# Kernel optimization log

Hardware: AMD Instinct MI355X
Metric: run time of the kernel (lower is better)

The kernel has to match this reference:

```python
import jax, jax.numpy as jnp
import numpy as np

B, C_IN, H, W = 128, 2, 64, 64
K = 50  # value-iteration steps


def _conv(x, w, b=None):
    # NCHW input, OIHW weights, stride 1, SAME padding (odd kernel)
    y = jax.lax.conv_general_dilated(
        x, w, window_strides=(1, 1), padding='SAME',
        dimension_numbers=('NCHW', 'OIHW', 'NCHW'))
    if b is not None:
        y = y + b[None, :, None, None]
    return y


def setup_inputs() -> dict:
    key = jax.random.key(0)
    ks = jax.random.split(key, 10)
    pos_x = jax.random.randint(ks[0], (B,), 0, H, dtype=jnp.int32)
    pos_y = jax.random.randint(ks[1], (B,), 0, W, dtype=jnp.int32)
    # channel 0 encodes agent position (single >0 entry); channel 1 is the obstacle/goal map
    ch0 = jnp.zeros((B, H, W), jnp.float32).at[jnp.arange(B), pos_x, pos_y].set(1.0)
    ch1 = jax.random.normal(ks[2], (B, H, W), jnp.float32)
    x = jnp.stack([ch0, ch1], axis=1)  # [B, 2, H, W]
    sc = lambda *s: 1.0 / np.sqrt(np.prod(s[1:])) if len(s) > 1 else 0.1
    h_w = jax.random.normal(ks[3], (150, C_IN, 3, 3), jnp.float32) * sc(150, C_IN, 3, 3)
    h_b = jax.random.normal(ks[4], (150,), jnp.float32) * 0.1
    r_w = jax.random.normal(ks[5], (1, 150, 3, 3), jnp.float32) * sc(1, 150, 3, 3)
    r_b = jax.random.normal(ks[6], (1,), jnp.float32) * 0.1
    q_w = jax.random.normal(ks[7], (10, 2, 3, 3), jnp.float32) * sc(10, 2, 3, 3)
    q_b = jax.random.normal(ks[8], (10,), jnp.float32) * 0.1
    fc_w = jax.random.normal(ks[9], (8, 10), jnp.float32) * sc(8, 10)
    return {'x': x, 'pos_x': pos_x, 'pos_y': pos_y,
            'h_w': h_w, 'h_b': h_b, 'r_w': r_w, 'r_b': r_b,
            'q_w': q_w, 'q_b': q_b, 'fc_w': fc_w}


def reference(x, pos_x, pos_y, h_w, h_b, r_w, r_b, q_w, q_b, fc_w):
    h = _conv(x, h_w, h_b)            # [B, 150, H, W]
    r = _conv(h, r_w, r_b)            # [B, 1, H, W]
    v0 = jnp.zeros_like(r)

    def vi_step(v, _):
        q = _conv(jnp.concatenate([r, v], axis=1), q_w, q_b)  # [B, 10, H, W]
        return jnp.max(q, axis=1, keepdims=True), None

    v, _ = jax.lax.scan(vi_step, v0, None, length=K)
    q = _conv(jnp.concatenate([r, v], axis=1), q_w, q_b)      # [B, 10, H, W]
    q_at = q[jnp.arange(q.shape[0]), :, pos_x, pos_y]         # [B, 10]
    return q_at @ fc_w.T                                       # [B, 8]
```

## Files before the change

### kernel.cpp

```cpp
#include <hip/hip_runtime.h>

#define K_ITERS 50

__global__ void vin_setup(const float* __restrict__ h_w, const float* __restrict__ h_b,
                          const float* __restrict__ r_w, float* __restrict__ ws) {
    int t = threadIdx.x;
    if (t < 162) {
        int i = t / 81, rem = t % 81, dq = rem / 9, ds = rem % 9;
        float s = 0.f;
        for (int m = 0; m < 150; ++m)
            s = fmaf(r_w[m * 9 + dq], h_w[(m * 2 + i) * 9 + ds], s);
        ws[t] = s;
    } else if (t < 171) {
        int dq = t - 162;
        float s = 0.f;
        for (int m = 0; m < 150; ++m)
            s = fmaf(r_w[m * 9 + dq], h_b[m], s);
        ws[t] = s;
    }
}

#define SR_OFF 9248
#define SW_OFF 13736
#define LDS_TOT 14178

__device__ __forceinline__ void vi_step(const float* __restrict__ cur, float* __restrict__ nxt,
                                        int row, int col0,
                                        const float (&qr)[10][8], const float (&qwv)[10][9]) {
    float nb[3][12];
#pragma unroll
    for (int dy = 0; dy < 3; ++dy) {
#pragma unroll
        for (int j = 0; j < 3; ++j) {
            float4 v = *(const float4*)&cur[(row + dy) * 68 + col0 + 4 * j];
            nb[dy][4 * j + 0] = v.x; nb[dy][4 * j + 1] = v.y;
            nb[dy][4 * j + 2] = v.z; nb[dy][4 * j + 3] = v.w;
        }
    }
    float vmax[8];
#pragma unroll
    for (int c = 0; c < 10; ++c) {
#pragma unroll
        for (int p = 0; p < 8; ++p) {
            float acc = qr[c][p];
#pragma unroll
            for (int ky = 0; ky < 3; ++ky)
#pragma unroll
                for (int kx = 0; kx < 3; ++kx)
                    acc = fmaf(qwv[c][ky * 3 + kx], nb[ky][p + kx], acc);
            vmax[p] = (c == 0) ? acc : fmaxf(vmax[p], acc);
        }
    }
#pragma unroll
    for (int p = 0; p < 8; ++p)
        nxt[(row + 1) * 68 + col0 + 1 + p] = vmax[p];
}

__launch_bounds__(512)
__global__ void vin_main(const float* __restrict__ x,
                         const int* __restrict__ pos_x, const int* __restrict__ pos_y,
                         const float* __restrict__ q_w, const float* __restrict__ q_b,
                         const float* __restrict__ fc_w, const float* __restrict__ r_b,
                         const float* __restrict__ ws, float* __restrict__ out) {
    __shared__ __align__(16) float S[LDS_TOT];
    const int tid = threadIdx.x;
    const int b = blockIdx.x;
    const int row = tid >> 3;
    const int col0 = (tid & 7) << 3;
    float* SW = S + SW_OFF;

    float4 z4 = make_float4(0.f, 0.f, 0.f, 0.f);
    for (int i = tid; i < 3434; i += 512) ((float4*)S)[i] = z4;
    for (int i = tid; i < 171; i += 512) SW[i] = ws[i];
    for (int i = tid; i < 180; i += 512) SW[171 + i] = q_w[i];
    if (tid < 10) SW[351 + tid] = q_b[tid];
    for (int i = tid; i < 80; i += 512) SW[361 + i] = fc_w[i];
    if (tid == 0) SW[441] = r_b[0];
    __syncthreads();

    {
        const float4* xg = (const float4*)(x + (size_t)b * 8192);
        for (int i = tid; i < 2048; i += 512) {
            float4 v = xg[i];
            int ch = i >> 10, rem = i & 1023;
            int y = rem >> 4, xc = (rem & 15) << 2;
            float* dst = S + ch * 4624 + (y + 2) * 68 + xc + 2;
            dst[0] = v.x; dst[1] = v.y; dst[2] = v.z; dst[3] = v.w;
        }
    }
    __syncthreads();

    {
        float xb0[5][12], xb1[5][12];
        const float* X0 = S;
        const float* X1 = S + 4624;
#pragma unroll
        for (int dy = 0; dy < 5; ++dy) {
#pragma unroll
            for (int j = 0; j < 3; ++j) {
                float4 a = *(const float4*)&X0[(row + dy) * 68 + col0 + 4 * j];
                xb0[dy][4 * j + 0] = a.x; xb0[dy][4 * j + 1] = a.y;
                xb0[dy][4 * j + 2] = a.z; xb0[dy][4 * j + 3] = a.w;
                float4 c = *(const float4*)&X1[(row + dy) * 68 + col0 + 4 * j];
                xb1[dy][4 * j + 0] = c.x; xb1[dy][4 * j + 1] = c.y;
                xb1[dy][4 * j + 2] = c.z; xb1[dy][4 * j + 3] = c.w;
            }
        }
        float racc[8];
        float rbv = SW[441];
#pragma unroll
        for (int p = 0; p < 8; ++p) racc[p] = rbv;
#pragma unroll
        for (int dqy = 0; dqy < 3; ++dqy) {
            bool rowok = (row + dqy >= 1) && (row + dqy <= 64);
#pragma unroll
            for (int dqx = 0; dqx < 3; ++dqx) {
                int dq = dqy * 3 + dqx;
                float rh = SW[162 + dq];
                float w20[9], w21[9];
#pragma unroll
                for (int ds = 0; ds < 9; ++ds) {
                    w20[ds] = SW[dq * 9 + ds];
                    w21[ds] = SW[81 + dq * 9 + ds];
                }
#pragma unroll
                for (int p = 0; p < 8; ++p) {
                    float t = rh;
#pragma unroll
                    for (int dsy = 0; dsy < 3; ++dsy)
#pragma unroll
                        for (int dsx = 0; dsx < 3; ++dsx) {
                            int ds = dsy * 3 + dsx;
                            t = fmaf(w20[ds], xb0[dqy + dsy][p + dqx + dsx], t);
                            t = fmaf(w21[ds], xb1[dqy + dsy][p + dqx + dsx], t);
                        }
                    int qx = col0 + p + dqx - 1;
                    bool ok = rowok && (qx >= 0) && (qx < 64);
                    racc[p] += ok ? t : 0.f;
                }
            }
        }
        float* SR = S + SR_OFF;
#pragma unroll
        for (int p = 0; p < 8; ++p)
            SR[(row + 1) * 68 + col0 + 1 + p] = racc[p];
    }
    __syncthreads();

    float qr[10][8];
    float qwv[10][9];
    {
        float rnb[3][12];
        const float* SR = S + SR_OFF;
#pragma unroll
        for (int dy = 0; dy < 3; ++dy) {
#pragma unroll
            for (int j = 0; j < 3; ++j) {
                float4 v = *(const float4*)&SR[(row + dy) * 68 + col0 + 4 * j];
                rnb[dy][4 * j + 0] = v.x; rnb[dy][4 * j + 1] = v.y;
                rnb[dy][4 * j + 2] = v.z; rnb[dy][4 * j + 3] = v.w;
            }
        }
#pragma unroll
        for (int c = 0; c < 10; ++c) {
            float qbc = SW[351 + c];
            float w[9];
#pragma unroll
            for (int j = 0; j < 9; ++j) w[j] = SW[171 + c * 18 + j];
#pragma unroll
            for (int p = 0; p < 8; ++p) {
                float acc = qbc;
#pragma unroll
                for (int ky = 0; ky < 3; ++ky)
#pragma unroll
                    for (int kx = 0; kx < 3; ++kx)
                        acc = fmaf(w[ky * 3 + kx], rnb[ky][p + kx], acc);
                qr[c][p] = acc;
            }
        }
#pragma unroll
        for (int c = 0; c < 10; ++c)
#pragma unroll
            for (int j = 0; j < 9; ++j) qwv[c][j] = SW[171 + c * 18 + 9 + j];
        for (int i = tid; i < 2312; i += 512) ((float4*)S)[i] = z4;
    }
    __syncthreads();

    float* vA = S;
    float* vB = S + 4624;
#pragma unroll 1
    for (int k = 0; k < K_ITERS / 2; ++k) {
        vi_step(vA, vB, row, col0, qr, qwv);
        __syncthreads();
        vi_step(vB, vA, row, col0, qr, qwv);
        __syncthreads();
    }

    int pr = pos_x[b], pc = pos_y[b];
    if (row == pr && (pc >> 3) == (tid & 7)) {
        int p = pc & 7;
        float qf[10];
#pragma unroll
        for (int c = 0; c < 10; ++c) {
            float acc = qr[c][p];
#pragma unroll
            for (int ky = 0; ky < 3; ++ky)
#pragma unroll
                for (int kx = 0; kx < 3; ++kx)
                    acc = fmaf(qwv[c][3 * ky + kx], vA[(pr + ky) * 68 + pc + kx], acc);
            qf[c] = acc;
        }
#pragma unroll
        for (int o = 0; o < 8; ++o) {
            float s = 0.f;
#pragma unroll
            for (int c = 0; c < 10; ++c) s = fmaf(SW[361 + o * 10 + c], qf[c], s);
            out[b * 8 + o] = s;
        }
    }
}

extern "C" void kernel_launch(void* const* d_in, const int* in_sizes, int n_in,
                              void* d_out, int out_size, void* d_ws, size_t ws_size,
                              hipStream_t stream) {
    const float* x     = (const float*)d_in[0];
    const int*   pos_x = (const int*)d_in[1];
    const int*   pos_y = (const int*)d_in[2];
    const float* h_w   = (const float*)d_in[3];
    const float* h_b   = (const float*)d_in[4];
    const float* r_w   = (const float*)d_in[5];
    const float* r_b   = (const float*)d_in[6];
    const float* q_w   = (const float*)d_in[7];
    const float* q_b   = (const float*)d_in[8];
    const float* fc_w  = (const float*)d_in[9];
    float* ws  = (float*)d_ws;
    float* out = (float*)d_out;

    vin_setup<<<1, 192, 0, stream>>>(h_w, h_b, r_w, ws);
    vin_main<<<128, 512, 0, stream>>>(x, pos_x, pos_y, q_w, q_b, fc_w, r_b, ws, out);
}
```

Baseline: 198.7 us.

## Split each image across two blocks with global-memory halo exchange per iteration

Each image is now processed by two workgroups, each owning 32 rows, so 256 blocks run instead of 128 and more CUs are occupied. Each thread computes 4 columns instead of 8. The two halves swap boundary rows through double-buffered global slots and synchronise every value-iteration step with acquire/release flag spin-waits. This adds inter-block synchronisation latency on every step, and correctness relies on both partner blocks being co-resident.

```diff
diff --git a/kernel.cpp b/kernel.cpp
--- a/kernel.cpp
+++ b/kernel.cpp
@@ -1,6 +1,16 @@
 #include <hip/hip_runtime.h>
 
-#define K_ITERS 50
+#define KI 50
+#define STR 72
+
+#define VA_OFF 0
+#define VB_OFF 2448
+#define X0_OFF 0
+#define R_OFF 4896
+#define X1_OFF 7344
+#define W_OFF 10080
+#define LDS_TOT 10522
+
 
 __global__ void vin_setup(const float* __restrict__ h_w, const float* __restrict__ h_b,
                           const float* __restrict__ r_w, float* __restrict__ ws) {
@@ -18,147 +28,132 @@
             s = fmaf(r_w[m * 9 + dq], h_b[m], s);
         ws[t] = s;
     }
+    int* flags = (int*)ws + 256;
+    if (t < 256) flags[t] = 0;
 }
 
-#define SR_OFF 9248
-#define SW_OFF 13736
-#define LDS_TOT 14178
-
-__device__ __forceinline__ void vi_step(const float* __restrict__ cur, float* __restrict__ nxt,
-                                        int row, int col0,
-                                        const float (&qr)[10][8], const float (&qwv)[10][9]) {
-    float nb[3][12];
-#pragma unroll
-    for (int dy = 0; dy < 3; ++dy) {
-#pragma unroll
-        for (int j = 0; j < 3; ++j) {
-            float4 v = *(const float4*)&cur[(row + dy) * 68 + col0 + 4 * j];
-            nb[dy][4 * j + 0] = v.x; nb[dy][4 * j + 1] = v.y;
-            nb[dy][4 * j + 2] = v.z; nb[dy][4 * j + 3] = v.w;
-        }
-    }
-    float vmax[8];
-#pragma unroll
-    for (int c = 0; c < 10; ++c) {
-#pragma unroll
-        for (int p = 0; p < 8; ++p) {
-            float acc = qr[c][p];
-#pragma unroll
-            for (int ky = 0; ky < 3; ++ky)
-#pragma unroll
-                for (int kx = 0; kx < 3; ++kx)
-                    acc = fmaf(qwv[c][ky * 3 + kx], nb[ky][p + kx], acc);
-            vmax[p] = (c == 0) ? acc : fmaxf(vmax[p], acc);
-        }
-    }
-#pragma unroll
-    for (int p = 0; p < 8; ++p)
-        nxt[(row + 1) * 68 + col0 + 1 + p] = vmax[p];
-}
-
-__launch_bounds__(512)
+__launch_bounds__(512, 2)
 __global__ void vin_main(const float* __restrict__ x,
                          const int* __restrict__ pos_x, const int* __restrict__ pos_y,
                          const float* __restrict__ q_w, const float* __restrict__ q_b,
                          const float* __restrict__ fc_w, const float* __restrict__ r_b,
-                         const float* __restrict__ ws, float* __restrict__ out) {
+                         float* __restrict__ ws, float* __restrict__ out) {
     __shared__ __align__(16) float S[LDS_TOT];
     const int tid = threadIdx.x;
-    const int b = blockIdx.x;
-    const int row = tid >> 3;
-    const int col0 = (tid & 7) << 3;
-    float* SW = S + SW_OFF;
+    const int img = blockIdx.x & 127;
+    const int hf  = blockIdx.x >> 7;
+    const int base = hf << 5;
+    const int rr = tid >> 4;
+    const int c4 = (tid & 15) << 2;
+    float* SW = S + W_OFF;
+    int* flags = (int*)ws + 256;
+    float* slots = ws + 1024;
+    const int self = img * 2 + hf;
+    const int partner = img * 2 + (1 - hf);
 
     float4 z4 = make_float4(0.f, 0.f, 0.f, 0.f);
-    for (int i = tid; i < 3434; i += 512) ((float4*)S)[i] = z4;
+    for (int i = tid; i < 2520; i += 512) ((float4*)S)[i] = z4;
     for (int i = tid; i < 171; i += 512) SW[i] = ws[i];
     for (int i = tid; i < 180; i += 512) SW[171 + i] = q_w[i];
     if (tid < 10) SW[351 + tid] = q_b[tid];
     for (int i = tid; i < 80; i += 512) SW[361 + i] = fc_w[i];
     if (tid == 0) SW[441] = r_b[0];
+    if (tid < 36) ((float4*)(slots + self * 144))[tid] = z4;
     __syncthreads();
 
     {
-        const float4* xg = (const float4*)(x + (size_t)b * 8192);
-        for (int i = tid; i < 2048; i += 512) {
-            float4 v = xg[i];
-            int ch = i >> 10, rem = i & 1023;
-            int y = rem >> 4, xc = (rem & 15) << 2;
-            float* dst = S + ch * 4624 + (y + 2) * 68 + xc + 2;
-            dst[0] = v.x; dst[1] = v.y; dst[2] = v.z; dst[3] = v.w;
-        }
-    }
-    __syncthreads();
-
-    {
-        float xb0[5][12], xb1[5][12];
-        const float* X0 = S;
-        const float* X1 = S + 4624;
-#pragma unroll
-        for (int dy = 0; dy < 5; ++dy) {
-#pragma unroll
-            for (int j = 0; j < 3; ++j) {
-                float4 a = *(const float4*)&X0[(row + dy) * 68 + col0 + 4 * j];
-                xb0[dy][4 * j + 0] = a.x; xb0[dy][4 * j + 1] = a.y;
-                xb0[dy][4 * j + 2] = a.z; xb0[dy][4 * j + 3] = a.w;
-                float4 c = *(const float4*)&X1[(row + dy) * 68 + col0 + 4 * j];
-                xb1[dy][4 * j + 0] = c.x; xb1[dy][4 * j + 1] = c.y;
-                xb1[dy][4 * j + 2] = c.z; xb1[dy][4 * j + 3] = c.w;
-            }
-        }
-        float racc[8];
-        float rbv = SW[441];
-#pragma unroll
-        for (int p = 0; p < 8; ++p) racc[p] = rbv;
-#pragma unroll
-        for (int dqy = 0; dqy < 3; ++dqy) {
-            bool rowok = (row + dqy >= 1) && (row + dqy <= 64);
-#pragma unroll
-            for (int dqx = 0; dqx < 3; ++dqx) {
-                int dq = dqy * 3 + dqx;
-                float rh = SW[162 + dq];
-                float w20[9], w21[9];
-#pragma unroll
-                for (int ds = 0; ds < 9; ++ds) {
-                    w20[ds] = SW[dq * 9 + ds];
-                    w21[ds] = SW[81 + dq * 9 + ds];
-                }
-#pragma unroll
-                for (int p = 0; p < 8; ++p) {
-                    float t = rh;
-#pragma unroll
-                    for (int dsy = 0; dsy < 3; ++dsy)
-#pragma unroll
-                        for (int dsx = 0; dsx < 3; ++dsx) {
-                            int ds = dsy * 3 + dsx;
-                            t = fmaf(w20[ds], xb0[dqy + dsy][p + dqx + dsx], t);
-                            t = fmaf(w21[ds], xb1[dqy + dsy][p + dqx + dsx], t);
+        const int gstart = hf ? 29 : 0;
+        for (int i = tid; i < 1120; i += 512) {
+            int ch = i / 560, rem = i - ch * 560;
+            int rowi = rem >> 4, cx = (rem & 15) << 2;
+            int g = gstart + rowi;
+            int lx = g - base + 3;
+            float4 v = *(const float4*)(x + (size_t)img * 8192 + ch * 4096 + g * 64 + cx);
+            *(float4*)&S[(ch ? X1_OFF : X0_OFF) + lx * STR + 4 + cx] = v;
+        }
+    }
+    __syncthreads();
+
+    for (int pass = 0; pass < 2; ++pass) {
+        int lr = rr + (pass << 5);
+        if (lr < 34) {
+            int g = base - 1 + lr;
+            if ((unsigned)g <= 63u) {
+                float tacc[9][4];
+#pragma unroll
+                for (int dq = 0; dq < 9; ++dq) {
+                    float rh = SW[162 + dq];
+#pragma unroll
+                    for (int p = 0; p < 4; ++p) tacc[dq][p] = rh;
+                }
+#pragma unroll
+                for (int ch = 0; ch < 2; ++ch) {
+                    float xb[5][12];
+                    const float* X = S + (ch ? X1_OFF : X0_OFF);
+#pragma unroll
+                    for (int dy = 0; dy < 5; ++dy) {
+#pragma unroll
+                        for (int j = 0; j < 3; ++j) {
+                            float4 a = *(const float4*)&X[(lr + dy) * STR + c4 + 4 * j];
+                            xb[dy][4 * j + 0] = a.x; xb[dy][4 * j + 1] = a.y;
+                            xb[dy][4 * j + 2] = a.z; xb[dy][4 * j + 3] = a.w;
                         }
-                    int qx = col0 + p + dqx - 1;
-                    bool ok = rowok && (qx >= 0) && (qx < 64);
-                    racc[p] += ok ? t : 0.f;
-                }
-            }
-        }
-        float* SR = S + SR_OFF;
-#pragma unroll
-        for (int p = 0; p < 8; ++p)
-            SR[(row + 1) * 68 + col0 + 1 + p] = racc[p];
-    }
-    __syncthreads();
-
-    float qr[10][8];
+                    }
+#pragma unroll
+                    for (int dqy = 0; dqy < 3; ++dqy)
+#pragma unroll
+                        for (int dqx = 0; dqx < 3; ++dqx) {
+                            int dq = dqy * 3 + dqx;
+                            float w[9];
+#pragma unroll
+                            for (int ds = 0; ds < 9; ++ds) w[ds] = SW[ch * 81 + dq * 9 + ds];
+#pragma unroll
+                            for (int p = 0; p < 4; ++p) {
+                                float t = tacc[dq][p];
+#pragma unroll
+                                for (int dsy = 0; dsy < 3; ++dsy)
+#pragma unroll
+                                    for (int dsx = 0; dsx < 3; ++dsx)
+                                        t = fmaf(w[dsy * 3 + dsx], xb[dqy + dsy][p + dqx + dsx + 2], t);
+                                tacc[dq][p] = t;
+                            }
+                        }
+                }
+                float rbv = SW[441];
+                float racc[4] = {rbv, rbv, rbv, rbv};
+#pragma unroll
+                for (int dqy = 0; dqy < 3; ++dqy) {
+                    int qy = g + dqy - 1;
+                    bool rok = (unsigned)qy <= 63u;
+#pragma unroll
+                    for (int dqx = 0; dqx < 3; ++dqx) {
+                        int dq = dqy * 3 + dqx;
+#pragma unroll
+                        for (int p = 0; p < 4; ++p) {
+                            int qx = c4 + p + dqx - 1;
+                            racc[p] += (rok && (unsigned)qx <= 63u) ? tacc[dq][p] : 0.f;
+                        }
+                    }
+                }
+                *(float4*)&S[R_OFF + lr * STR + 4 + c4] =
+                    make_float4(racc[0], racc[1], racc[2], racc[3]);
+            }
+        }
+    }
+    __syncthreads();
+
+    float qr[10][4];
     float qwv[10][9];
     {
         float rnb[3][12];
-        const float* SR = S + SR_OFF;
-#pragma unroll
-        for (int dy = 0; dy < 3; ++dy) {
+        const float* SR = S + R_OFF;
+#pragma unroll
+        for (int ky = 0; ky < 3; ++ky) {
 #pragma unroll
             for (int j = 0; j < 3; ++j) {
-                float4 v = *(const float4*)&SR[(row + dy) * 68 + col0 + 4 * j];
-                rnb[dy][4 * j + 0] = v.x; rnb[dy][4 * j + 1] = v.y;
-                rnb[dy][4 * j + 2] = v.z; rnb[dy][4 * j + 3] = v.w;
+                float4 a = *(const float4*)&SR[(rr + ky) * STR + c4 + 4 * j];
+                rnb[ky][4 * j + 0] = a.x; rnb[ky][4 * j + 1] = a.y;
+                rnb[ky][4 * j + 2] = a.z; rnb[ky][4 * j + 3] = a.w;
             }
         }
 #pragma unroll
@@ -168,13 +163,13 @@
 #pragma unroll
             for (int j = 0; j < 9; ++j) w[j] = SW[171 + c * 18 + j];
 #pragma unroll
-            for (int p = 0; p < 8; ++p) {
+            for (int p = 0; p < 4; ++p) {
                 float acc = qbc;
 #pragma unroll
                 for (int ky = 0; ky < 3; ++ky)
 #pragma unroll
                     for (int kx = 0; kx < 3; ++kx)
-                        acc = fmaf(w[ky * 3 + kx], rnb[ky][p + kx], acc);
+                        acc = fmaf(w[ky * 3 + kx], rnb[ky][p + kx + 3], acc);
                 qr[c][p] = acc;
             }
         }
@@ -182,40 +177,100 @@
         for (int c = 0; c < 10; ++c)
 #pragma unroll
             for (int j = 0; j < 9; ++j) qwv[c][j] = SW[171 + c * 18 + 9 + j];
-        for (int i = tid; i < 2312; i += 512) ((float4*)S)[i] = z4;
-    }
-    __syncthreads();
-
-    float* vA = S;
-    float* vB = S + 4624;
+        for (int i = tid; i < 1224; i += 512) ((float4*)S)[i] = z4;
+    }
+    __syncthreads();
+
+    const int bRR = hf ? 0 : 31;
+    const bool isB = (rr == bRR);
+    const int haloDy = hf ? 0 : 2;
+    float* cur = S + VA_OFF;
+    float* nxt = S + VB_OFF;
 #pragma unroll 1
-    for (int k = 0; k < K_ITERS / 2; ++k) {
-        vi_step(vA, vB, row, col0, qr, qwv);
+    for (int k = 1; k <= KI; ++k) {
+        if (tid == 0) {
+            while (__hip_atomic_load(flags + partner, __ATOMIC_ACQUIRE,
+                                     __HIP_MEMORY_SCOPE_AGENT) < k - 1)
+                __builtin_amdgcn_s_sleep(1);
+        }
         __syncthreads();
-        vi_step(vB, vA, row, col0, qr, qwv);
+        const float* slotR = slots + (partner * 2 + ((k - 1) & 1)) * STR;
+        float nb[3][12];
+#pragma unroll
+        for (int dy = 0; dy < 3; ++dy) {
+            float4 a0, a1, a2;
+            if (isB && dy == haloDy && k > 1) {
+                const float4* gp = (const float4*)(slotR + c4);
+                a0 = gp[0]; a1 = gp[1]; a2 = gp[2];
+            } else {
+                const float* lp = cur + (rr + dy) * STR + c4;
+                a0 = *(const float4*)lp; a1 = *(const float4*)(lp + 4); a2 = *(const float4*)(lp + 8);
+            }
+            nb[dy][0] = a0.x; nb[dy][1] = a0.y; nb[dy][2]  = a0.z; nb[dy][3]  = a0.w;
+            nb[dy][4] = a1.x; nb[dy][5] = a1.y; nb[dy][6]  = a1.z; nb[dy][7]  = a1.w;
+            nb[dy][8] = a2.x; nb[dy][9] = a2.y; nb[dy][10] = a2.z; nb[dy][11] = a2.w;
+        }
+        float vmax[4];
+#pragma unroll
+        for (int c = 0; c < 10; ++c) {
+#pragma unroll
+            for (int p = 0; p < 4; ++p) {
+                float acc = qr[c][p];
+#pragma unroll
+                for (int ky = 0; ky < 3; ++ky)
+#pragma unroll
+                    for (int kx = 0; kx < 3; ++kx)
+                        acc = fmaf(qwv[c][ky * 3 + kx], nb[ky][p + kx + 3], acc);
+                vmax[p] = c ? fmaxf(vmax[p], acc) : acc;
+            }
+        }
+        float4 vv = make_float4(vmax[0], vmax[1], vmax[2], vmax[3]);
+        *(float4*)&nxt[(rr + 1) * STR + 4 + c4] = vv;
+        if (isB) *(float4*)(slots + (self * 2 + (k & 1)) * STR + 4 + c4) = vv;
         __syncthreads();
-    }
-
-    int pr = pos_x[b], pc = pos_y[b];
-    if (row == pr && (pc >> 3) == (tid & 7)) {
-        int p = pc & 7;
-        float qf[10];
-#pragma unroll
-        for (int c = 0; c < 10; ++c) {
-            float acc = qr[c][p];
-#pragma unroll
-            for (int ky = 0; ky < 3; ++ky)
-#pragma unroll
-                for (int kx = 0; kx < 3; ++kx)
-                    acc = fmaf(qwv[c][3 * ky + kx], vA[(pr + ky) * 68 + pc + kx], acc);
-            qf[c] = acc;
-        }
-#pragma unroll
-        for (int o = 0; o < 8; ++o) {
-            float s = 0.f;
-#pragma unroll
-            for (int c = 0; c < 10; ++c) s = fmaf(SW[361 + o * 10 + c], qf[c], s);
-            out[b * 8 + o] = s;
+        if (tid == 0) {
+            __threadfence();
+            __hip_atomic_store(flags + self, k, __ATOMIC_RELEASE, __HIP_MEMORY_SCOPE_AGENT);
+        }
+        float* t = cur; cur = nxt; nxt = t;
+    }
+
+    if (tid == 0) {
+        while (__hip_atomic_load(flags + partner, __ATOMIC_ACQUIRE,
+                                 __HIP_MEMORY_SCOPE_AGENT) < KI)
+            __builtin_amdgcn_s_sleep(1);
+    }
+    __syncthreads();
+    int pr = pos_x[img], pc = pos_y[img];
+    if ((pr >> 5) == hf) {
+        int rloc = pr - base;
+        if (tid == rloc * 16 + (pc >> 2)) {
+            const float* slotF = slots + (partner * 2 + 0) * STR;
+            int p = pc & 3;
+            float qf[10];
+#pragma unroll
+            for (int c = 0; c < 10; ++c) {
+                float acc = qr[c][p];
+#pragma unroll
+                for (int ky = 0; ky < 3; ++ky) {
+                    int vr = rloc + ky;
+                    bool halo = hf ? (vr == 0) : (vr == 33);
+#pragma unroll
+                    for (int kx = 0; kx < 3; ++kx) {
+                        int off = 4 + pc + kx - 1;
+                        float vvv = halo ? slotF[off] : cur[vr * STR + off];
+                        acc = fmaf(qwv[c][ky * 3 + kx], vvv, acc);
+                    }
+                }
+                qf[c] = acc;
+            }
+#pragma unroll
+            for (int o = 0; o < 8; ++o) {
+                float s = 0.f;
+#pragma unroll
+                for (int c = 0; c < 10; ++c) s = fmaf(SW[361 + o * 10 + c], qf[c], s);
+                out[img * 8 + o] = s;
+            }
         }
     }
 }
@@ -236,6 +291,6 @@
     float* ws  = (float*)d_ws;
     float* out = (float*)d_out;
 
-    vin_setup<<<1, 192, 0, stream>>>(h_w, h_b, r_w, ws);
-    vin_main<<<128, 512, 0, stream>>>(x, pos_x, pos_y, q_w, q_b, fc_w, r_b, ws, out);
+    vin_setup<<<1, 512, 0, stream>>>(h_w, h_b, r_w, ws);
+    vin_main<<<256, 512, 0, stream>>>(x, pos_x, pos_y, q_w, q_b, fc_w, r_b, ws, out);
 }
```

Measured after the change: 583.3 us. 2.94x slower.

## Fuse weight-folding setup into main kernel and shift padded value layout

Applied to the files above, without the earlier changes.

Removes the separate single-block setup kernel and has each block compute the folded r∘h conv weights itself, overlapping that work with the input tile load. The padded value grids gain an extra column of offset so that value writes become aligned float2 stores instead of scalar stores, and the input scatter into LDS also uses float2 stores. It also adds a min-blocks hint to the launch bounds. The cost is that every block redundantly performs the 150-term reductions from global memory, which delays the first barrier.

```diff
diff --git a/kernel.cpp b/kernel.cpp
--- a/kernel.cpp
+++ b/kernel.cpp
@@ -1,41 +1,25 @@
 #include <hip/hip_runtime.h>
 
-#define K_ITERS 50
-
-__global__ void vin_setup(const float* __restrict__ h_w, const float* __restrict__ h_b,
-                          const float* __restrict__ r_w, float* __restrict__ ws) {
-    int t = threadIdx.x;
-    if (t < 162) {
-        int i = t / 81, rem = t % 81, dq = rem / 9, ds = rem % 9;
-        float s = 0.f;
-        for (int m = 0; m < 150; ++m)
-            s = fmaf(r_w[m * 9 + dq], h_w[(m * 2 + i) * 9 + ds], s);
-        ws[t] = s;
-    } else if (t < 171) {
-        int dq = t - 162;
-        float s = 0.f;
-        for (int m = 0; m < 150; ++m)
-            s = fmaf(r_w[m * 9 + dq], h_b[m], s);
-        ws[t] = s;
-    }
-}
-
-#define SR_OFF 9248
-#define SW_OFF 13736
+#define KI 50
+
+#define X1_OFF 4624
+#define R_OFF 9248
+#define W_OFF 13736
 #define LDS_TOT 14178
 
 __device__ __forceinline__ void vi_step(const float* __restrict__ cur, float* __restrict__ nxt,
-                                        int row, int col0,
+                                        int row, int c0,
                                         const float (&qr)[10][8], const float (&qwv)[10][9]) {
     float nb[3][12];
 #pragma unroll
     for (int dy = 0; dy < 3; ++dy) {
-#pragma unroll
-        for (int j = 0; j < 3; ++j) {
-            float4 v = *(const float4*)&cur[(row + dy) * 68 + col0 + 4 * j];
-            nb[dy][4 * j + 0] = v.x; nb[dy][4 * j + 1] = v.y;
-            nb[dy][4 * j + 2] = v.z; nb[dy][4 * j + 3] = v.w;
-        }
+        const float* lp = cur + (row + dy) * 68 + c0;
+        float4 a0 = *(const float4*)lp;
+        float4 a1 = *(const float4*)(lp + 4);
+        float4 a2 = *(const float4*)(lp + 8);
+        nb[dy][0] = a0.x; nb[dy][1] = a0.y; nb[dy][2]  = a0.z; nb[dy][3]  = a0.w;
+        nb[dy][4] = a1.x; nb[dy][5] = a1.y; nb[dy][6]  = a1.z; nb[dy][7]  = a1.w;
+        nb[dy][8] = a2.x; nb[dy][9] = a2.y; nb[dy][10] = a2.z; nb[dy][11] = a2.w;
     }
     float vmax[8];
 #pragma unroll
@@ -47,35 +31,32 @@
             for (int ky = 0; ky < 3; ++ky)
 #pragma unroll
                 for (int kx = 0; kx < 3; ++kx)
-                    acc = fmaf(qwv[c][ky * 3 + kx], nb[ky][p + kx], acc);
-            vmax[p] = (c == 0) ? acc : fmaxf(vmax[p], acc);
-        }
-    }
-#pragma unroll
-    for (int p = 0; p < 8; ++p)
-        nxt[(row + 1) * 68 + col0 + 1 + p] = vmax[p];
+                    acc = fmaf(qwv[c][ky * 3 + kx], nb[ky][p + kx + 1], acc);
+            vmax[p] = c ? fmaxf(vmax[p], acc) : acc;
+        }
+    }
+    float* wp = nxt + (row + 1) * 68 + 2 + c0;
+#pragma unroll
+    for (int j = 0; j < 4; ++j)
+        *(float2*)(wp + 2 * j) = make_float2(vmax[2 * j], vmax[2 * j + 1]);
 }
 
-__launch_bounds__(512)
+__launch_bounds__(512, 2)
 __global__ void vin_main(const float* __restrict__ x,
                          const int* __restrict__ pos_x, const int* __restrict__ pos_y,
+                         const float* __restrict__ h_w, const float* __restrict__ h_b,
+                         const float* __restrict__ r_w, const float* __restrict__ r_b,
                          const float* __restrict__ q_w, const float* __restrict__ q_b,
-                         const float* __restrict__ fc_w, const float* __restrict__ r_b,
-                         const float* __restrict__ ws, float* __restrict__ out) {
+                         const float* __restrict__ fc_w, float* __restrict__ out) {
     __shared__ __align__(16) float S[LDS_TOT];
     const int tid = threadIdx.x;
     const int b = blockIdx.x;
     const int row = tid >> 3;
-    const int col0 = (tid & 7) << 3;
-    float* SW = S + SW_OFF;
+    const int c0 = (tid & 7) << 3;
+    float* SW = S + W_OFF;
 
     float4 z4 = make_float4(0.f, 0.f, 0.f, 0.f);
     for (int i = tid; i < 3434; i += 512) ((float4*)S)[i] = z4;
-    for (int i = tid; i < 171; i += 512) SW[i] = ws[i];
-    for (int i = tid; i < 180; i += 512) SW[171 + i] = q_w[i];
-    if (tid < 10) SW[351 + tid] = q_b[tid];
-    for (int i = tid; i < 80; i += 512) SW[361 + i] = fc_w[i];
-    if (tid == 0) SW[441] = r_b[0];
     __syncthreads();
 
     {
@@ -85,23 +66,45 @@
             int ch = i >> 10, rem = i & 1023;
             int y = rem >> 4, xc = (rem & 15) << 2;
             float* dst = S + ch * 4624 + (y + 2) * 68 + xc + 2;
-            dst[0] = v.x; dst[1] = v.y; dst[2] = v.z; dst[3] = v.w;
-        }
+            *(float2*)dst       = make_float2(v.x, v.y);
+            *(float2*)(dst + 2) = make_float2(v.z, v.w);
+        }
+    }
+    if (tid < 162) {
+        int i = tid / 81, rem = tid % 81, dq = rem / 9, ds = rem % 9;
+        float s = 0.f;
+        for (int m = 0; m < 150; ++m)
+            s = fmaf(r_w[m * 9 + dq], h_w[(m * 2 + i) * 9 + ds], s);
+        SW[tid] = s;
+    } else if (tid < 171) {
+        int dq = tid - 162;
+        float s = 0.f;
+        for (int m = 0; m < 150; ++m)
+            s = fmaf(r_w[m * 9 + dq], h_b[m], s);
+        SW[tid] = s;
+    } else if (tid < 351) {
+        SW[tid] = q_w[tid - 171];
+    } else if (tid < 361) {
+        SW[tid] = q_b[tid - 351];
+    } else if (tid < 441) {
+        SW[tid] = fc_w[tid - 361];
+    } else if (tid == 441) {
+        SW[441] = r_b[0];
     }
     __syncthreads();
 
     {
         float xb0[5][12], xb1[5][12];
         const float* X0 = S;
-        const float* X1 = S + 4624;
+        const float* X1 = S + X1_OFF;
 #pragma unroll
         for (int dy = 0; dy < 5; ++dy) {
 #pragma unroll
             for (int j = 0; j < 3; ++j) {
-                float4 a = *(const float4*)&X0[(row + dy) * 68 + col0 + 4 * j];
+                float4 a = *(const float4*)&X0[(row + dy) * 68 + c0 + 4 * j];
                 xb0[dy][4 * j + 0] = a.x; xb0[dy][4 * j + 1] = a.y;
                 xb0[dy][4 * j + 2] = a.z; xb0[dy][4 * j + 3] = a.w;
-                float4 c = *(const float4*)&X1[(row + dy) * 68 + col0 + 4 * j];
+                float4 c = *(const float4*)&X1[(row + dy) * 68 + c0 + 4 * j];
                 xb1[dy][4 * j + 0] = c.x; xb1[dy][4 * j + 1] = c.y;
                 xb1[dy][4 * j + 2] = c.z; xb1[dy][4 * j + 3] = c.w;
             }
@@ -134,16 +137,15 @@
                             t = fmaf(w20[ds], xb0[dqy + dsy][p + dqx + dsx], t);
                             t = fmaf(w21[ds], xb1[dqy + dsy][p + dqx + dsx], t);
                         }
-                    int qx = col0 + p + dqx - 1;
+                    int qx = c0 + p + dqx - 1;
                     bool ok = rowok && (qx >= 0) && (qx < 64);
                     racc[p] += ok ? t : 0.f;
                 }
             }
         }
-        float* SR = S + SR_OFF;
 #pragma unroll
         for (int p = 0; p < 8; ++p)
-            SR[(row + 1) * 68 + col0 + 1 + p] = racc[p];
+            S[R_OFF + (row + 1) * 68 + 2 + c0 + p] = racc[p];
     }
     __syncthreads();
 
@@ -151,15 +153,16 @@
     float qwv[10][9];
     {
         float rnb[3][12];
-        const float* SR = S + SR_OFF;
-#pragma unroll
-        for (int dy = 0; dy < 3; ++dy) {
-#pragma unroll
-            for (int j = 0; j < 3; ++j) {
-                float4 v = *(const float4*)&SR[(row + dy) * 68 + col0 + 4 * j];
-                rnb[dy][4 * j + 0] = v.x; rnb[dy][4 * j + 1] = v.y;
-                rnb[dy][4 * j + 2] = v.z; rnb[dy][4 * j + 3] = v.w;
-            }
+        const float* SR = S + R_OFF;
+#pragma unroll
+        for (int ky = 0; ky < 3; ++ky) {
+            const float* lp = SR + (row + ky) * 68 + c0;
+            float4 a0 = *(const float4*)lp;
+            float4 a1 = *(const float4*)(lp + 4);
+            float4 a2 = *(const float4*)(lp + 8);
+            rnb[ky][0] = a0.x; rnb[ky][1] = a0.y; rnb[ky][2]  = a0.z; rnb[ky][3]  = a0.w;
+            rnb[ky][4] = a1.x; rnb[ky][5] = a1.y; rnb[ky][6]  = a1.z; rnb[ky][7]  = a1.w;
+            rnb[ky][8] = a2.x; rnb[ky][9] = a2.y; rnb[ky][10] = a2.z; rnb[ky][11] = a2.w;
         }
 #pragma unroll
         for (int c = 0; c < 10; ++c) {
@@ -174,7 +177,7 @@
                 for (int ky = 0; ky < 3; ++ky)
 #pragma unroll
                     for (int kx = 0; kx < 3; ++kx)
-                        acc = fmaf(w[ky * 3 + kx], rnb[ky][p + kx], acc);
+                        acc = fmaf(w[ky * 3 + kx], rnb[ky][p + kx + 1], acc);
                 qr[c][p] = acc;
             }
         }
@@ -187,12 +190,12 @@
     __syncthreads();
 
     float* vA = S;
-    float* vB = S + 4624;
+    float* vB = S + X1_OFF;
 #pragma unroll 1
-    for (int k = 0; k < K_ITERS / 2; ++k) {
-        vi_step(vA, vB, row, col0, qr, qwv);
+    for (int k = 0; k < KI / 2; ++k) {
+        vi_step(vA, vB, row, c0, qr, qwv);
         __syncthreads();
-        vi_step(vB, vA, row, col0, qr, qwv);
+        vi_step(vB, vA, row, c0, qr, qwv);
         __syncthreads();
     }
 
@@ -207,7 +210,7 @@
             for (int ky = 0; ky < 3; ++ky)
 #pragma unroll
                 for (int kx = 0; kx < 3; ++kx)
-                    acc = fmaf(qwv[c][3 * ky + kx], vA[(pr + ky) * 68 + pc + kx], acc);
+                    acc = fmaf(qwv[c][3 * ky + kx], vA[(pr + ky) * 68 + pc + 1 + kx], acc);
             qf[c] = acc;
         }
 #pragma unroll
@@ -233,9 +236,8 @@
     const float* q_w   = (const float*)d_in[7];
     const float* q_b   = (const float*)d_in[8];
     const float* fc_w  = (const float*)d_in[9];
-    float* ws  = (float*)d_ws;
     float* out = (float*)d_out;
 
-    vin_setup<<<1, 192, 0, stream>>>(h_w, h_b, r_w, ws);
-    vin_main<<<128, 512, 0, stream>>>(x, pos_x, pos_y, q_w, q_b, fc_w, r_b, ws, out);
+    vin_main<<<128, 512, 0, stream>>>(x, pos_x, pos_y, h_w, h_b, r_w, r_b,
+                                      q_w, q_b, fc_w, out);
 }
```

Result: slower. 219.7 us (+10.6%).
